# Kernel tuning notes

Hardware: AMD Instinct MI355X
Metric: run time of the kernel (lower is better)

## Reference

```python
import jax, jax.numpy as jnp
import numpy as np

LN_EPS = 1e-5  # torch LayerNorm default


def setup_inputs() -> dict:
    key = jax.random.key(0)
    k1, k2, k3 = jax.random.split(key, 3)
    B, L, D = 8, 2048, 1024
    CS, CD = 8192, 16
    x = jax.random.normal(k1, (B, L, D), dtype=jnp.float32)
    # xavier_uniform for Linear(dim, codebook_dim): bound = sqrt(6/(fan_in+fan_out))
    bound = float(np.sqrt(6.0 / (D + CD)))
    W = jax.random.uniform(k2, (CD, D), dtype=jnp.float32, minval=-bound, maxval=bound)
    codebook = jax.random.normal(k3, (CS, CD), dtype=jnp.float32)
    return {"x": x, "W": W, "codebook": codebook}


def reference(x, W, codebook):
    # random projection: (B,L,D) @ (D,CD) -> (B,L,CD)
    z = jnp.einsum("bld,cd->blc", x, W)
    # LayerNorm over last dim, no affine
    mu = jnp.mean(z, axis=-1, keepdims=True)
    var = jnp.mean(jnp.square(z - mu), axis=-1, keepdims=True)
    z = (z - mu) / jnp.sqrt(var + LN_EPS)
    # squared euclidean distance via matmul decomposition (avoids (B,L,CS,CD) tensor):
    # ||z - c||^2 = ||z||^2 - 2 z.c + ||c||^2 ; argmin is identical to argmin of the norm
    z_sq = jnp.sum(jnp.square(z), axis=-1, keepdims=True)        # (B,L,1)
    c_sq = jnp.sum(jnp.square(codebook), axis=-1)                # (CS,)
    d2 = z_sq - 2.0 * jnp.einsum("blc,kc->blk", z, codebook) + c_sq  # (B,L,CS)
    codes = jnp.argmin(d2, axis=-1)                              # (B,L) int32
    return codes
```

## Files before the change

kernel.cpp:

```cpp
#include <hip/hip_runtime.h>
#include <math.h>

#define D      1024
#define CD     16
#define CS     8192
#define ROWS   16384
#define LN_EPS 1e-5f
#define KCHUNK 512
#define NCHUNK (CS / KCHUNK)

typedef __attribute__((ext_vector_type(8))) short short8;
typedef __attribute__((ext_vector_type(4))) float f32x4;
typedef __attribute__((ext_vector_type(16))) float f32x16;

__device__ inline unsigned short bf16_rne(float v) {
    unsigned u = __float_as_uint(v);
    unsigned r = u + 0x7FFFu + ((u >> 16) & 1u);
    return (unsigned short)(r >> 16);
}
__device__ inline short8 ld8(const unsigned short* p) { return *(const short8*)p; }

__device__ inline void split3(float v, unsigned short& a, unsigned short& b, unsigned short& c) {
    unsigned u = __float_as_uint(v);
    unsigned r = u + 0x7FFFu + ((u >> 16) & 1u);
    a = (unsigned short)(r >> 16);
    float r1 = v - __uint_as_float(r & 0xFFFF0000u);
    unsigned u1 = __float_as_uint(r1);
    unsigned r1b = u1 + 0x7FFFu + ((u1 >> 16) & 1u);
    b = (unsigned short)(r1b >> 16);
    float r2 = r1 - __uint_as_float(r1b & 0xFFFF0000u);
    c = bf16_rne(r2);
}

__global__ __launch_bounds__(256) void pack_all(const float* __restrict__ W,
                                                const float* __restrict__ cb,
                                                unsigned short* __restrict__ wb,
                                                unsigned short* __restrict__ cbp,
                                                float* __restrict__ nhc)
{
    const int t = threadIdx.x;
    if (blockIdx.x < 32) {
        int k = blockIdx.x * 256 + t;
        const float* c = cb + (long)k * CD;
        unsigned short* o = cbp + (long)k * 48;
        float csq = 0.f;
        #pragma unroll
        for (int d = 0; d < 16; ++d) {
            float v = c[d];
            csq = fmaf(v, v, csq);
            unsigned short h0, h1, h2;
            split3(v, h0, h1, h2);
            o[d] = h0; o[16 + d] = h1; o[32 + d] = h2;
        }
        nhc[k] = -0.5f * csq;
    } else {
        int tid = (blockIdx.x - 32) * 256 + t;
        int gk   = tid / 192;
        int rem  = tid % 192;
        int term = rem >> 6;
        int L    = rem & 63;
        int n = L & 15, q = L >> 4;
        const float* src = W + n * D + gk * 32 + q * 8;
        unsigned short* dst = wb + (size_t)tid * 8;
        #pragma unroll
        for (int j = 0; j < 8; ++j) {
            unsigned short h0, h1, h2;
            split3(src[j], h0, h1, h2);
            dst[j] = term == 0 ? h0 : (term == 1 ? h1 : h2);
        }
    }
}

__global__ __launch_bounds__(256, 4) void proj_ln(const float* __restrict__ x,
                                                  const unsigned short* __restrict__ wb,
                                                  unsigned short* __restrict__ zp)
{
    __shared__ float part[3][64][4];
    const int t = threadIdx.x;
    const int L = t & 63;
    const int kq = t >> 6;
    const int rt = blockIdx.x;
    const int n = L & 15, q = L >> 4;

    const float* xrow = x + (size_t)(rt * 16 + n) * D + kq * 256 + q * 8;
    const unsigned short* wbase = wb + (size_t)(kq * 8) * 1536;

    f32x4 acc0 = {0.f, 0.f, 0.f, 0.f};
    f32x4 acc1 = {0.f, 0.f, 0.f, 0.f};
    #pragma unroll
    for (int kk = 0; kk < 8; ++kk) {
        float4 xa = *(const float4*)(xrow + kk * 32);
        float4 xb = *(const float4*)(xrow + kk * 32 + 4);
        const unsigned short* wp = wbase + (size_t)kk * 1536 + L * 8;
        short8 w0 = ld8(wp);
        short8 w1 = ld8(wp + 512);
        short8 w2 = ld8(wp + 1024);
        float vs[8] = {xa.x, xa.y, xa.z, xa.w, xb.x, xb.y, xb.z, xb.w};
        short8 x0, x1, x2;
        #pragma unroll
        for (int j = 0; j < 8; ++j) {
            unsigned short h0, h1, h2;
            split3(vs[j], h0, h1, h2);
            x0[j] = (short)h0; x1[j] = (short)h1; x2[j] = (short)h2;
        }
        acc0 = __builtin_amdgcn_mfma_f32_16x16x32_bf16(x0, w0, acc0, 0, 0, 0);
        acc1 = __builtin_amdgcn_mfma_f32_16x16x32_bf16(x0, w1, acc1, 0, 0, 0);
        acc0 = __builtin_amdgcn_mfma_f32_16x16x32_bf16(x1, w0, acc0, 0, 0, 0);
        acc1 = __builtin_amdgcn_mfma_f32_16x16x32_bf16(x1, w1, acc1, 0, 0, 0);
        acc0 = __builtin_amdgcn_mfma_f32_16x16x32_bf16(x0, w2, acc0, 0, 0, 0);
        acc1 = __builtin_amdgcn_mfma_f32_16x16x32_bf16(x2, w0, acc1, 0, 0, 0);
    }

    if (kq != 0) {
        #pragma unroll
        for (int r = 0; r < 4; ++r) part[kq - 1][L][r] = acc0[r] + acc1[r];
    }
    __syncthreads();
    if (kq == 0) {
        #pragma unroll
        for (int r = 0; r < 4; ++r) {
            float zv = acc0[r] + acc1[r] + part[0][L][r] + part[1][L][r] + part[2][L][r];
            float s = zv;
            for (int m = 1; m < 16; m <<= 1) s += __shfl_xor(s, m, 64);
            float mu = s * (1.f / 16.f);
            float dd = zv - mu;
            float v2 = dd * dd;
            for (int m = 1; m < 16; m <<= 1) v2 += __shfl_xor(v2, m, 64);
            float var = v2 * (1.f / 16.f);
            float zn = dd / sqrtf(var + LN_EPS);
            unsigned short h0, h1, h2;
            split3(zn, h0, h1, h2);
            unsigned short* zr = zp + (size_t)(rt * 16 + q * 4 + r) * 48;
            zr[n] = h0; zr[16 + n] = h1; zr[32 + n] = h2;
        }
    }
}

__global__ __launch_bounds__(512, 4) void dist_argmin(const unsigned short* __restrict__ zp,
                                                      const unsigned short* __restrict__ cbp,
                                                      const float* __restrict__ nhc,
                                                      float* __restrict__ pbest,
                                                      int* __restrict__ pidx)
{
    __shared__ __align__(16) unsigned short cl[KCHUNK * 48];
    __shared__ float ql[KCHUNK];
    const int t = threadIdx.x;
    const int kbase = blockIdx.y * KCHUNK;

    {
        float4* dst = (float4*)cl;
        const float4* src = (const float4*)(cbp + (size_t)kbase * 48);
        #pragma unroll
        for (int i = 0; i < 6; ++i) dst[t + i * 512] = src[t + i * 512];
        if (t < KCHUNK / 4) ((float4*)ql)[t] = ((const float4*)(nhc + kbase))[t];
    }
    __syncthreads();

    const int L = t & 63;
    const int w = t >> 6;
    const int c31 = L & 31;
    const int half = L >> 5;

    const int rt = blockIdx.x * 8 + w;
    const unsigned short* zr = zp + (size_t)(rt * 32 + c31) * 48 + half * 8;
    short8 a0 = ld8(zr);
    short8 a1 = ld8(zr + 16);
    short8 a2 = ld8(zr + 32);

    float best[16];
    int   bi[16];
    #pragma unroll
    for (int r = 0; r < 16; ++r) { best[r] = -INFINITY; bi[r] = 0; }

    #pragma unroll 2
    for (int tt = 0; tt < KCHUNK / 32; ++tt) {
        const unsigned short* cp = cl + (size_t)(tt * 32 + c31) * 48 + half * 8;
        short8 b0 = ld8(cp);
        short8 b1 = ld8(cp + 16);
        short8 b2 = ld8(cp + 32);
        float bneg = ql[tt * 32 + c31];
        int code = kbase + tt * 32 + c31;
        f32x16 acc;
        #pragma unroll
        for (int r = 0; r < 16; ++r) acc[r] = bneg;
        acc = __builtin_amdgcn_mfma_f32_32x32x16_bf16(a0, b0, acc, 0, 0, 0);
        acc = __builtin_amdgcn_mfma_f32_32x32x16_bf16(a1, b1, acc, 0, 0, 0);
        acc = __builtin_amdgcn_mfma_f32_32x32x16_bf16(a1, b0, acc, 0, 0, 0);
        acc = __builtin_amdgcn_mfma_f32_32x32x16_bf16(a0, b1, acc, 0, 0, 0);
        acc = __builtin_amdgcn_mfma_f32_32x32x16_bf16(a2, b0, acc, 0, 0, 0);
        acc = __builtin_amdgcn_mfma_f32_32x32x16_bf16(a0, b2, acc, 0, 0, 0);
        #pragma unroll
        for (int r = 0; r < 16; ++r)
            if (acc[r] > best[r]) { best[r] = acc[r]; bi[r] = code; }
    }

    #pragma unroll
    for (int mask = 1; mask < 32; mask <<= 1) {
        #pragma unroll
        for (int r = 0; r < 16; ++r) {
            float s2 = __shfl_xor(best[r], mask, 64);
            int   i2 = __shfl_xor(bi[r], mask, 64);
            if (s2 > best[r] || (s2 == best[r] && i2 < bi[r])) {
                best[r] = s2; bi[r] = i2;
            }
        }
    }
    if (c31 == 0) {
        #pragma unroll
        for (int r = 0; r < 16; ++r) {
            int row = rt * 32 + (r & 3) + 8 * (r >> 2) + 4 * half;
            pbest[(size_t)row * NCHUNK + blockIdx.y] = best[r];
            pidx [(size_t)row * NCHUNK + blockIdx.y] = bi[r];
        }
    }
}

__global__ __launch_bounds__(256) void merge_argmin(const float* __restrict__ pbest,
                                                    const int* __restrict__ pidx,
                                                    int* __restrict__ out)
{
    const long row = (long)blockIdx.x * 256 + threadIdx.x;
    float best = -INFINITY;
    int   bi   = 0;
    #pragma unroll
    for (int i = 0; i < NCHUNK; ++i) {
        float s = pbest[row * NCHUNK + i];
        if (s > best) { best = s; bi = pidx[row * NCHUNK + i]; }
    }
    out[row] = bi;
}

extern "C" void kernel_launch(void* const* d_in, const int* in_sizes, int n_in,
                              void* d_out, int out_size, void* d_ws, size_t ws_size,
                              hipStream_t stream)
{
    const float* x  = (const float*)d_in[0];
    const float* W  = (const float*)d_in[1];
    const float* cb = (const float*)d_in[2];
    int* out = (int*)d_out;

    char* ws = (char*)d_ws;
    unsigned short* zp  = (unsigned short*)ws;
    unsigned short* cbp = (unsigned short*)(ws + 0x180000);
    float* nhc  = (float*)(ws + 0x240000);
    unsigned short* wb = (unsigned short*)(ws + 0x248000);
    float* pbest = (float*)(ws + 0x260000);
    int*   pidx  = (int*)  (ws + 0x360000);

    pack_all<<<56, 256, 0, stream>>>(W, cb, wb, cbp, nhc);
    proj_ln <<<ROWS / 16, 256, 0, stream>>>(x, wb, zp);
    dist_argmin<<<dim3(ROWS / 256, NCHUNK), 512, 0, stream>>>(zp, cbp, nhc, pbest, pidx);
    merge_argmin<<<ROWS / 256, 256, 0, stream>>>(pbest, pidx, out);
}
```

Baseline: 145.9 us.

## Pre-tile codebook into MFMA fragment layout and stream it from global memory

The pack kernel now writes the split bf16 codebook in a per-chunk, per-tile layout that matches the MFMA B-fragment lane order, so each lane reads contiguous 16-byte vectors. The distance kernel drops its shared-memory staging of the codebook chunk and the barrier, loading fragments straight from global/L2 instead. This also removes the 48 KB of LDS per block, which can raise occupancy. It records the winning tile index rather than the full code inside the loop and rebuilds the code afterwards. The trade-off is that every wave in a block rereads the same chunk from cache instead of from LDS.

```diff
diff --git a/kernel.cpp b/kernel.cpp
--- a/kernel.cpp
+++ b/kernel.cpp
@@ -42,15 +42,31 @@
     if (blockIdx.x < 32) {
         int k = blockIdx.x * 256 + t;
         const float* c = cb + (long)k * CD;
-        unsigned short* o = cbp + (long)k * 48;
+        int ci  = k >> 9;
+        int tt  = (k >> 5) & 15;
+        int c31 = k & 31;
+        unsigned short* base = cbp + (size_t)ci * 24576 + tt * 1536;
         float csq = 0.f;
+        unsigned short h0[16], h1[16], h2[16];
         #pragma unroll
         for (int d = 0; d < 16; ++d) {
             float v = c[d];
             csq = fmaf(v, v, csq);
-            unsigned short h0, h1, h2;
-            split3(v, h0, h1, h2);
-            o[d] = h0; o[16 + d] = h1; o[32 + d] = h2;
+            split3(v, h0[d], h1[d], h2[d]);
+        }
+        #pragma unroll
+        for (int h = 0; h < 2; ++h) {
+            short8 v0, v1, v2;
+            #pragma unroll
+            for (int j = 0; j < 8; ++j) {
+                v0[j] = (short)h0[h * 8 + j];
+                v1[j] = (short)h1[h * 8 + j];
+                v2[j] = (short)h2[h * 8 + j];
+            }
+            int lofs = (h * 32 + c31) * 8;
+            *(short8*)(base + lofs)        = v0;
+            *(short8*)(base + 512 + lofs)  = v1;
+            *(short8*)(base + 1024 + lofs) = v2;
         }
         nhc[k] = -0.5f * csq;
     } else {
@@ -142,20 +158,8 @@
                                                       float* __restrict__ pbest,
                                                       int* __restrict__ pidx)
 {
-    __shared__ __align__(16) unsigned short cl[KCHUNK * 48];
-    __shared__ float ql[KCHUNK];
     const int t = threadIdx.x;
     const int kbase = blockIdx.y * KCHUNK;
-
-    {
-        float4* dst = (float4*)cl;
-        const float4* src = (const float4*)(cbp + (size_t)kbase * 48);
-        #pragma unroll
-        for (int i = 0; i < 6; ++i) dst[t + i * 512] = src[t + i * 512];
-        if (t < KCHUNK / 4) ((float4*)ql)[t] = ((const float4*)(nhc + kbase))[t];
-    }
-    __syncthreads();
-
     const int L = t & 63;
     const int w = t >> 6;
     const int c31 = L & 31;
@@ -167,19 +171,21 @@
     short8 a1 = ld8(zr + 16);
     short8 a2 = ld8(zr + 32);
 
+    const unsigned short* cstream = cbp + (size_t)blockIdx.y * 24576 + L * 8;
+    const float* nh = nhc + kbase + c31;
+
     float best[16];
-    int   bi[16];
-    #pragma unroll
-    for (int r = 0; r < 16; ++r) { best[r] = -INFINITY; bi[r] = 0; }
+    int   bt[16];
+    #pragma unroll
+    for (int r = 0; r < 16; ++r) { best[r] = -INFINITY; bt[r] = 0; }
 
     #pragma unroll 2
     for (int tt = 0; tt < KCHUNK / 32; ++tt) {
-        const unsigned short* cp = cl + (size_t)(tt * 32 + c31) * 48 + half * 8;
-        short8 b0 = ld8(cp);
-        short8 b1 = ld8(cp + 16);
-        short8 b2 = ld8(cp + 32);
-        float bneg = ql[tt * 32 + c31];
-        int code = kbase + tt * 32 + c31;
+        const unsigned short* bp = cstream + tt * 1536;
+        short8 b0 = ld8(bp);
+        short8 b1 = ld8(bp + 512);
+        short8 b2 = ld8(bp + 1024);
+        float bneg = nh[tt * 32];
         f32x16 acc;
         #pragma unroll
         for (int r = 0; r < 16; ++r) acc[r] = bneg;
@@ -191,8 +197,12 @@
         acc = __builtin_amdgcn_mfma_f32_32x32x16_bf16(a0, b2, acc, 0, 0, 0);
         #pragma unroll
         for (int r = 0; r < 16; ++r)
-            if (acc[r] > best[r]) { best[r] = acc[r]; bi[r] = code; }
-    }
+            if (acc[r] > best[r]) { best[r] = acc[r]; bt[r] = tt; }
+    }
+
+    int bi[16];
+    #pragma unroll
+    for (int r = 0; r < 16; ++r) bi[r] = kbase + bt[r] * 32 + c31;
 
     #pragma unroll
     for (int mask = 1; mask < 32; mask <<= 1) {
```

Measured after the change: 151.1 us. 1.04x slower.
